# Performance work log

Measured on AMD Instinct MI355X. Metric: run time of the kernel, lower is better.

## Reference

```python
import jax, jax.numpy as jnp
import numpy as np

BATCH, HORIZON, NU, NY, K = 524288, 50, 4, 4, 32


def setup_inputs() -> dict:
    key = jax.random.key(0)
    ks = jax.random.split(key, 4)
    u = jax.random.normal(ks[0], (BATCH, HORIZON, NU), dtype=jnp.float32)
    y0 = jax.random.normal(ks[1], (BATCH, NY), dtype=jnp.float32)
    Wh = jax.random.normal(ks[2], (NU + NY, K), dtype=jnp.float32) * 0.3
    bh = jnp.zeros((K,), dtype=jnp.float32)
    Wo = jax.random.normal(ks[3], (K, 1), dtype=jnp.float32) * 0.3
    bo = jnp.zeros((1,), dtype=jnp.float32)
    return {"u": u, "y0": y0, "Wh": Wh, "bh": bh, "Wo": Wo, "bo": bo}


def reference(u, y0, Wh, bh, Wo, bo):
    u_t = jnp.transpose(u, (1, 0, 2))  # (T, B, NU) for scan

    def step(y_pred, ut):
        x = jnp.concatenate([ut, y_pred], axis=1)          # (B, NU+NY)
        h = jnp.tanh(x @ Wh + bh)                          # (B, K)
        pred = h @ Wo + bo                                 # (B, 1)
        # roll(shift=1)[:,1:] then prepend pred == drop last, prepend pred
        y_new = jnp.concatenate([pred, y_pred[:, :-1]], axis=1)
        return y_new, pred

    _, preds = jax.lax.scan(step, y0, u_t)  # preds: (T, B, 1)
    return jnp.transpose(preds, (1, 0, 2))  # (B, T, 1)
```

## Files before the change

kernel.cpp:

```cpp
#include <hip/hip_runtime.h>

#define T_HORIZON 50
#define NU 4
#define NY 4
#define KH 32
#define BPB 64

typedef float v2f __attribute__((ext_vector_type(2)));

__device__ __forceinline__ v2f fma2(v2f a, v2f b, v2f c) {
    return __builtin_elementwise_fma(a, b, c);
}

#define TANH_SCALE 2.88539008177792681472f

__global__ void stage_weights(const float* __restrict__ Whg,
                              const float* __restrict__ bhg,
                              const float* __restrict__ Wog,
                              float* __restrict__ ws) {
    int idx = threadIdx.x;
    if (idx < 320) {
        int jg = idx / 80, r = idx % 80, i = r / 8, k = r % 8;
        int j = jg + 4 * k;
        float v = (i < 8) ? Whg[i * KH + j] : (i == 8 ? bhg[j] : Wog[j]);
        ws[idx] = v;
    }
}

__global__ __launch_bounds__(256, 6) void rollout_kernel(
    const float* __restrict__ u,
    const float* __restrict__ y0g,
    const float* __restrict__ bog,
    const float* __restrict__ wsW,
    float* __restrict__ out)
{
    __shared__ __align__(16) float sOut[BPB * T_HORIZON];
    __shared__ float sRed[2][4][BPB];

    const int tid  = threadIdx.x;
    const int lane = tid & 63;
    const int jg = __builtin_amdgcn_readfirstlane(tid >> 6);

    const float* wb = wsW + jg * 80;
    v2f wh2[8][4], wor2[4];
#pragma unroll
    for (int i = 0; i < 8; ++i)
#pragma unroll
        for (int p = 0; p < 4; ++p)
            wh2[i][p] = *(const v2f*)(wb + i * 8 + 2 * p);
#pragma unroll
    for (int p = 0; p < 4; ++p)
        wor2[p] = *(const v2f*)(wb + 9 * 8 + 2 * p);
    const float bor = bog[0];

    float bhs[8];
#pragma unroll
    for (int k = 0; k < 8; ++k) bhs[k] = wb[8 * 8 + k];
#pragma unroll
    for (int k = 0; k < 8; ++k) asm volatile("" : "+v"(bhs[k]));
    v2f bh2[4];
#pragma unroll
    for (int p = 0; p < 4; ++p) bh2[p] = v2f{bhs[2 * p], bhs[2 * p + 1]};

    const v2f scale2 = {TANH_SCALE, TANH_SCALE};
    const v2f one2   = {1.0f, 1.0f};
    const v2f ntwo2  = {-2.0f, -2.0f};

    const int b = blockIdx.x * BPB + lane;
    const float4* ub = (const float4*)(u + (size_t)b * T_HORIZON * NU);
    float4 yv = *(const float4*)(y0g + (size_t)b * NY);
    float y1 = yv.x, y2 = yv.y, y3 = yv.z, y4 = yv.w;

    float4 un = ub[0];
    for (int t = 0; t < T_HORIZON; ++t) {
        float4 uc = un;
        if (t + 1 < T_HORIZON) un = ub[t + 1];

        v2f ux = {uc.x, uc.x}, uy = {uc.y, uc.y}, uz = {uc.z, uc.z}, uw = {uc.w, uc.w};
        v2f p1 = {y1, y1}, p2 = {y2, y2}, p3 = {y3, y3}, p4 = {y4, y4};

        float pcls = 0.0f;
#pragma unroll
        for (int p = 0; p < 4; ++p) {
            v2f a = fma2(ux, wh2[0][p], bh2[p]);
            a = fma2(uy, wh2[1][p], a);
            a = fma2(uz, wh2[2][p], a);
            a = fma2(uw, wh2[3][p], a);
            a = fma2(p1, wh2[4][p], a);
            a = fma2(p2, wh2[5][p], a);
            a = fma2(p3, wh2[6][p], a);
            a = fma2(p4, wh2[7][p], a);

            v2f s = a * scale2;
            float e0 = __builtin_amdgcn_exp2f(s.x);
            float e1 = __builtin_amdgcn_exp2f(s.y);
            v2f ep = v2f{e0, e1} + one2;
            v2f r  = {__builtin_amdgcn_rcpf(ep.x), __builtin_amdgcn_rcpf(ep.y)};
            v2f th = fma2(ntwo2, r, one2);
            v2f m  = th * wor2[p];
            pcls += m.x;
            pcls += m.y;
        }

        const int buf = t & 1;
        sRed[buf][jg][lane] = pcls;
        __syncthreads();
        float c0 = sRed[buf][0][lane];
        float c1 = sRed[buf][1][lane];
        float c2 = sRed[buf][2][lane];
        float c3 = sRed[buf][3][lane];
        float partial = (c0 + c1) + (c2 + c3);
        float pred = bor + partial;

        if (jg == 0) sOut[lane * T_HORIZON + t] = pred;

        y4 = y3; y3 = y2; y2 = y1; y1 = pred;
    }
    __syncthreads();

    const float4* s4 = (const float4*)sOut;
    float4* o4 = (float4*)(out + (size_t)blockIdx.x * BPB * T_HORIZON);
#pragma unroll
    for (int k = 0; k < 4; ++k) {
        int idx = k * 256 + tid;
        if (idx < (BPB * T_HORIZON) / 4) o4[idx] = s4[idx];
    }
}

extern "C" void kernel_launch(void* const* d_in, const int* in_sizes, int n_in,
                              void* d_out, int out_size, void* d_ws, size_t ws_size,
                              hipStream_t stream) {
    const float* u   = (const float*)d_in[0];
    const float* y0g = (const float*)d_in[1];
    const float* Whg = (const float*)d_in[2];
    const float* bhg = (const float*)d_in[3];
    const float* Wog = (const float*)d_in[4];
    const float* bog = (const float*)d_in[5];
    float* out = (float*)d_out;
    float* ws  = (float*)d_ws;

    stage_weights<<<1, 320, 0, stream>>>(Whg, bhg, Wog, ws);

    const int B = in_sizes[1] / NY;
    dim3 grid(B / BPB), block(256);
    rollout_kernel<<<grid, block, 0, stream>>>(u, y0g, bog, ws, out);
}
```

Before: 335.1 us.

## Pack two batch rows per thread into packed-FP32 lanes

New measurement: 369.1 us. +10.1%, slower.

```diff
diff --git a/kernel.cpp b/kernel.cpp
--- a/kernel.cpp
+++ b/kernel.cpp
@@ -4,13 +4,14 @@
 #define NU 4
 #define NY 4
 #define KH 32
-#define BPB 64
+#define BPB 128
 
 typedef float v2f __attribute__((ext_vector_type(2)));
 
 __device__ __forceinline__ v2f fma2(v2f a, v2f b, v2f c) {
     return __builtin_elementwise_fma(a, b, c);
 }
+__device__ __forceinline__ v2f splat(float s) { return v2f{s, s}; }
 
 #define TANH_SCALE 2.88539008177792681472f
 
@@ -27,7 +28,7 @@
     }
 }
 
-__global__ __launch_bounds__(256, 6) void rollout_kernel(
+__global__ __launch_bounds__(256, 4) void rollout_kernel(
     const float* __restrict__ u,
     const float* __restrict__ y0g,
     const float* __restrict__ bog,
@@ -35,22 +36,21 @@
     float* __restrict__ out)
 {
     __shared__ __align__(16) float sOut[BPB * T_HORIZON];
-    __shared__ float sRed[2][4][BPB];
+    __shared__ v2f sRed[2][4][64];
 
     const int tid  = threadIdx.x;
     const int lane = tid & 63;
     const int jg = __builtin_amdgcn_readfirstlane(tid >> 6);
 
     const float* wb = wsW + jg * 80;
-    v2f wh2[8][4], wor2[4];
+    float wh[8][8], wor[8];
 #pragma unroll
     for (int i = 0; i < 8; ++i)
 #pragma unroll
-        for (int p = 0; p < 4; ++p)
-            wh2[i][p] = *(const v2f*)(wb + i * 8 + 2 * p);
+        for (int k = 0; k < 8; ++k)
+            wh[i][k] = wb[i * 8 + k];
 #pragma unroll
-    for (int p = 0; p < 4; ++p)
-        wor2[p] = *(const v2f*)(wb + 9 * 8 + 2 * p);
+    for (int k = 0; k < 8; ++k) wor[k] = wb[9 * 8 + k];
     const float bor = bog[0];
 
     float bhs[8];
@@ -58,38 +58,37 @@
     for (int k = 0; k < 8; ++k) bhs[k] = wb[8 * 8 + k];
 #pragma unroll
     for (int k = 0; k < 8; ++k) asm volatile("" : "+v"(bhs[k]));
-    v2f bh2[4];
-#pragma unroll
-    for (int p = 0; p < 4; ++p) bh2[p] = v2f{bhs[2 * p], bhs[2 * p + 1]};
 
     const v2f scale2 = {TANH_SCALE, TANH_SCALE};
     const v2f one2   = {1.0f, 1.0f};
     const v2f ntwo2  = {-2.0f, -2.0f};
 
-    const int b = blockIdx.x * BPB + lane;
-    const float4* ub = (const float4*)(u + (size_t)b * T_HORIZON * NU);
-    float4 yv = *(const float4*)(y0g + (size_t)b * NY);
-    float y1 = yv.x, y2 = yv.y, y3 = yv.z, y4 = yv.w;
+    const int bA = blockIdx.x * BPB + lane;
+    const int bB = bA + 64;
+    const float4* ubA = (const float4*)(u + (size_t)bA * T_HORIZON * NU);
+    const float4* ubB = (const float4*)(u + (size_t)bB * T_HORIZON * NU);
+    float4 yA = *(const float4*)(y0g + (size_t)bA * NY);
+    float4 yB = *(const float4*)(y0g + (size_t)bB * NY);
+    v2f py1 = {yA.x, yB.x}, py2 = {yA.y, yB.y}, py3 = {yA.z, yB.z}, py4 = {yA.w, yB.w};
 
-    float4 un = ub[0];
+    float4 unA = ubA[0], unB = ubB[0];
     for (int t = 0; t < T_HORIZON; ++t) {
-        float4 uc = un;
-        if (t + 1 < T_HORIZON) un = ub[t + 1];
+        float4 uA = unA, uB = unB;
+        if (t + 1 < T_HORIZON) { unA = ubA[t + 1]; unB = ubB[t + 1]; }
 
-        v2f ux = {uc.x, uc.x}, uy = {uc.y, uc.y}, uz = {uc.z, uc.z}, uw = {uc.w, uc.w};
-        v2f p1 = {y1, y1}, p2 = {y2, y2}, p3 = {y3, y3}, p4 = {y4, y4};
+        v2f ux = {uA.x, uB.x}, uy = {uA.y, uB.y}, uz = {uA.z, uB.z}, uw = {uA.w, uB.w};
 
-        float pcls = 0.0f;
+        v2f pcls = {0.0f, 0.0f};
 #pragma unroll
-        for (int p = 0; p < 4; ++p) {
-            v2f a = fma2(ux, wh2[0][p], bh2[p]);
-            a = fma2(uy, wh2[1][p], a);
-            a = fma2(uz, wh2[2][p], a);
-            a = fma2(uw, wh2[3][p], a);
-            a = fma2(p1, wh2[4][p], a);
-            a = fma2(p2, wh2[5][p], a);
-            a = fma2(p3, wh2[6][p], a);
-            a = fma2(p4, wh2[7][p], a);
+        for (int k = 0; k < 8; ++k) {
+            v2f a = fma2(ux, splat(wh[0][k]), v2f{bhs[k], bhs[k]});
+            a = fma2(uy,  splat(wh[1][k]), a);
+            a = fma2(uz,  splat(wh[2][k]), a);
+            a = fma2(uw,  splat(wh[3][k]), a);
+            a = fma2(py1, splat(wh[4][k]), a);
+            a = fma2(py2, splat(wh[5][k]), a);
+            a = fma2(py3, splat(wh[6][k]), a);
+            a = fma2(py4, splat(wh[7][k]), a);
 
             v2f s = a * scale2;
             float e0 = __builtin_amdgcn_exp2f(s.x);
@@ -97,31 +96,33 @@
             v2f ep = v2f{e0, e1} + one2;
             v2f r  = {__builtin_amdgcn_rcpf(ep.x), __builtin_amdgcn_rcpf(ep.y)};
             v2f th = fma2(ntwo2, r, one2);
-            v2f m  = th * wor2[p];
-            pcls += m.x;
-            pcls += m.y;
+            v2f m  = th * splat(wor[k]);
+            pcls += m;
         }
 
         const int buf = t & 1;
         sRed[buf][jg][lane] = pcls;
         __syncthreads();
-        float c0 = sRed[buf][0][lane];
-        float c1 = sRed[buf][1][lane];
-        float c2 = sRed[buf][2][lane];
-        float c3 = sRed[buf][3][lane];
-        float partial = (c0 + c1) + (c2 + c3);
-        float pred = bor + partial;
+        v2f c0 = sRed[buf][0][lane];
+        v2f c1 = sRed[buf][1][lane];
+        v2f c2 = sRed[buf][2][lane];
+        v2f c3 = sRed[buf][3][lane];
+        v2f partial = (c0 + c1) + (c2 + c3);
+        v2f pred = v2f{bor, bor} + partial;
 
-        if (jg == 0) sOut[lane * T_HORIZON + t] = pred;
+        if (jg == 0) {
+            sOut[lane * T_HORIZON + t]        = pred.x;
+            sOut[(lane + 64) * T_HORIZON + t] = pred.y;
+        }
 
-        y4 = y3; y3 = y2; y2 = y1; y1 = pred;
+        py4 = py3; py3 = py2; py2 = py1; py1 = pred;
     }
     __syncthreads();
 
     const float4* s4 = (const float4*)sOut;
     float4* o4 = (float4*)(out + (size_t)blockIdx.x * BPB * T_HORIZON);
 #pragma unroll
-    for (int k = 0; k < 4; ++k) {
+    for (int k = 0; k < 7; ++k) {
         int idx = k * 256 + tid;
         if (idx < (BPB * T_HORIZON) / 4) o4[idx] = s4[idx];
     }
```
